# Kernel tuning notes

Hardware: AMD Instinct MI355X
Metric: run time of the kernel (lower is better)

The kernel has to match this reference:

```python
import jax, jax.numpy as jnp
import numpy as np

NU, NI, K, D, B = 100000, 50000, 100, 64, 8192


def setup_inputs() -> dict:
    key = jax.random.key(0)
    ks = jax.random.split(key, 16)
    s = lambda fan_in: np.sqrt(2.0 / fan_in)  # kaiming_normal-ish scale
    return {
        "user_emb": jax.random.normal(ks[0], (NU, D), jnp.float32) * s(D),
        "item_emb": jax.random.normal(ks[1], (NI, D), jnp.float32) * s(D),
        "user_scr_tensor": jax.random.uniform(ks[2], (NU, K), jnp.float32) / K,
        "item_scr_tensor": jax.random.uniform(ks[3], (NI, K), jnp.float32) / K,
        "w1": jax.random.normal(ks[4], (64, 128), jnp.float32) * s(128),
        "b1": jnp.zeros((64,), jnp.float32),
        "w2": jax.random.normal(ks[5], (64, 64), jnp.float32) * s(64),
        "b2": jnp.zeros((64,), jnp.float32),
        "w3": jax.random.normal(ks[6], (32, 64), jnp.float32) * s(64),
        "b3": jnp.zeros((32,), jnp.float32),
        "w4": jax.random.normal(ks[7], (32, 32), jnp.float32) * s(32),
        "b4": jnp.zeros((32,), jnp.float32),
        "w5": jax.random.normal(ks[8], (1, 32), jnp.float32) * s(32),
        "b5": jnp.zeros((1,), jnp.float32),
        "user_idx_tensor": jax.random.randint(ks[9], (NU, K), 0, NU, jnp.int32),
        "item_idx_tensor": jax.random.randint(ks[10], (NI, K), 0, NI, jnp.int32),
        "user_idxs": jax.random.randint(ks[11], (B,), 0, NU, jnp.int32),
        "item_idxs": jax.random.randint(ks[12], (B,), 0, NI, jnp.int32),
    }


def _scored_pool(idx_tensor, emb, scr, idxs):
    neighs = idx_tensor[idxs]          # [B, K]
    neigh_emb = emb[neighs]            # [B, K, D]
    neigh_scr = scr[neighs]            # [B, K, K]
    return jnp.einsum("bkj,bjd->bkd", neigh_scr, neigh_emb)


def reference(user_emb, item_emb, user_scr_tensor, item_scr_tensor,
              w1, b1, w2, b2, w3, b3, w4, b4, w5, b5,
              user_idx_tensor, item_idx_tensor, user_idxs, item_idxs):
    su = _scored_pool(user_idx_tensor, user_emb, user_scr_tensor, user_idxs)  # [B,K,D]
    si = _scored_pool(item_idx_tensor, item_emb, item_scr_tensor, item_idxs)  # [B,K,D]
    x = jnp.concatenate([su, si], axis=2)  # [B, K, 2D]
    x = jax.nn.relu(x @ w1.T + b1)
    x = jax.nn.relu(x @ w2.T + b2)
    x = jax.nn.relu(x @ w3.T + b3)
    x = jax.nn.relu(x @ w4.T + b4)
    x = jax.nn.sigmoid(x @ w5.T + b5)  # [B, K, 1]
    return jnp.mean(x, axis=-2).squeeze()  # [B]
```

## Files before the change

kernel.cpp:

```cpp
#include <hip/hip_runtime.h>
#include <hip/hip_bf16.h>
#include <math.h>

typedef __attribute__((ext_vector_type(8))) short short8;
typedef __attribute__((ext_vector_type(4))) float f32x4;

#define KN 100

#define W1_OFF 0
#define W2_OFF 8192
#define W3_OFF 12288
#define W4_OFF 14336
#define SCRU_OFF 16384
#define SCRI_OFF (SCRU_OFF + 100000 * 128)
#define EMBU_OFF (SCRI_OFF + 50000 * 128)
#define EMBI_OFF (EMBU_OFF + 100000 * 64)

#define ET_STRIDE 136
#define ETU_OFF 14336
#define ETI_OFF (14336 + 64 * ET_STRIDE)
#define S_TOT   (14336 + 2 * 64 * ET_STRIDE)

__device__ __forceinline__ unsigned short f2bf(float f) {
  __hip_bfloat16 h = __float2bfloat16(f);
  return __builtin_bit_cast(unsigned short, h);
}

__device__ __forceinline__ void st8(unsigned short* d, float4 a, float4 b) {
  short8 h;
  h[0] = (short)f2bf(a.x); h[1] = (short)f2bf(a.y);
  h[2] = (short)f2bf(a.z); h[3] = (short)f2bf(a.w);
  h[4] = (short)f2bf(b.x); h[5] = (short)f2bf(b.y);
  h[6] = (short)f2bf(b.z); h[7] = (short)f2bf(b.w);
  *reinterpret_cast<short8*>(d) = h;
}

__device__ __forceinline__ short8 pk2(f32x4 a, f32x4 b) {
  short8 h;
  h[0] = (short)f2bf(a[0]); h[1] = (short)f2bf(a[1]);
  h[2] = (short)f2bf(a[2]); h[3] = (short)f2bf(a[3]);
  h[4] = (short)f2bf(b[0]); h[5] = (short)f2bf(b[1]);
  h[6] = (short)f2bf(b[2]); h[7] = (short)f2bf(b[3]);
  return h;
}

#define PREP_UNITS (15360 + 2400000 + 1200000)
__global__ void prep(const float* __restrict__ w1, const float* __restrict__ w2,
                     const float* __restrict__ w3, const float* __restrict__ w4,
                     const float* __restrict__ uscr, const float* __restrict__ iscr,
                     const float* __restrict__ uemb, const float* __restrict__ iemb,
                     unsigned short* __restrict__ ws) {
  const float4 z4 = {0.f, 0.f, 0.f, 0.f};
  const int stride = gridDim.x * 256;
  for (int t = blockIdx.x * 256 + threadIdx.x; t < PREP_UNITS; t += stride) {
    if (t < 15360) {
      const float* src; int rel, o, i, kt, base;
      if (t < 8192)       { src = w1; rel = t;         o = rel >> 7; i = rel & 127; kt = 4; base = W1_OFF; }
      else if (t < 12288) { src = w2; rel = t - 8192;  o = rel >> 6; i = rel & 63;  kt = 2; base = W2_OFF; }
      else if (t < 14336) { src = w3; rel = t - 12288; o = rel >> 6; i = rel & 63;  kt = 2; base = W3_OFF; }
      else                { src = w4; rel = t - 14336; o = rel >> 5; i = rel & 31;  kt = 1; base = W4_OFF; }
      int n = o >> 4, l15 = o & 15, k = i >> 5;
      int quad = (i >> 2) & 3, s = ((i >> 4) & 1) * 4 + (i & 3);
      ws[base + ((n * kt + k) * 64 + quad * 16 + l15) * 8 + s] = f2bf(src[rel]);
      continue;
    }
    int rel = t - 15360;
    if (rel < 2400000) {
      const float* src; unsigned short* dst; int row, g;
      if (rel < 1600000) {
        row = rel >> 4; g = rel & 15;
        src = uscr + (size_t)row * 100;
        dst = ws + SCRU_OFF + (size_t)row * 128 + g * 8;
      } else {
        int q = rel - 1600000; row = q >> 4; g = q & 15;
        src = iscr + (size_t)row * 100;
        dst = ws + SCRI_OFF + (size_t)row * 128 + g * 8;
      }
      const int jb = 32 * (g >> 2) + 4 * (g & 3);
      float4 va = (jb <= 96) ? *reinterpret_cast<const float4*>(src + jb) : z4;
      float4 vb = (jb <= 80) ? *reinterpret_cast<const float4*>(src + jb + 16) : z4;
      st8(dst, va, vb);
      continue;
    }
    rel -= 2400000;
    {
      const float* src; unsigned short* dst; int row, g;
      if (rel < 800000) {
        row = rel >> 3; g = rel & 7;
        src = uemb + (size_t)row * 64;
        dst = ws + EMBU_OFF + (size_t)row * 64 + g * 8;
      } else {
        int q = rel - 800000; row = q >> 3; g = q & 7;
        src = iemb + (size_t)row * 64;
        dst = ws + EMBI_OFF + (size_t)row * 64 + g * 8;
      }
      float4 va = *reinterpret_cast<const float4*>(src + g * 8);
      float4 vb = *reinterpret_cast<const float4*>(src + g * 8 + 4);
      st8(dst, va, vb);
    }
  }
}

__device__ __forceinline__ void pool_mfma(const unsigned short* __restrict__ Sb,
                                          const short8* sb, int l15, int quad,
                                          short8& f0, short8& f1) {
  f32x4 acc[4];
#pragma unroll
  for (int po = 0; po < 4; ++po) acc[po] = (f32x4){0.f, 0.f, 0.f, 0.f};
#pragma unroll
  for (int k4 = 0; k4 < 4; ++k4) {
#pragma unroll
    for (int po = 0; po < 4; ++po) {
      const int row = po * 16 + l15;
      const int hw = row * ET_STRIDE + (((k4 * 4 + quad) ^ ((row >> 3) & 7)) << 3);
      short8 ea = *reinterpret_cast<const short8*>(Sb + hw);
      acc[po] = __builtin_amdgcn_mfma_f32_16x16x32_bf16(ea, sb[k4], acc[po], 0, 0, 0);
    }
  }
  f0 = pk2(acc[0], acc[1]);
  f1 = pk2(acc[2], acc[3]);
}

__device__ __forceinline__ void et_store(unsigned short* __restrict__ S,
                                         const unsigned int* ev, int w, int c,
                                         int half, int base) {
#pragma unroll
  for (int rr = 0; rr < 8; ++rr) {
    const int rbase = w + rr * 7;
    if (rbase < 50) {
      const int r0 = rbase * 2;
      const int p0 = ((r0 >> 5) << 5) | (((r0 >> 2) & 3) << 3) |
                     (((r0 >> 4) & 1) << 2) | (r0 & 3);
      const int sw = ((c >> 2) & 7) << 3;
      const int q = (2 * c + half) * ET_STRIDE + (p0 ^ sw);
      unsigned int v = ev[rr];
      unsigned int p = __shfl_xor(v, 32, 64);
      unsigned int d = half ? ((v & 0xffff0000u) | (p >> 16))
                            : ((v & 0x0000ffffu) | (p << 16));
      *reinterpret_cast<unsigned int*>(&S[base + q]) = d;
    }
  }
}

__launch_bounds__(448, 4)
__global__ void cnn_mfma9(
    const unsigned short* __restrict__ ws,
    const float* __restrict__ b1, const float* __restrict__ b2,
    const float* __restrict__ b3, const float* __restrict__ b4,
    const float* __restrict__ w5, const float* __restrict__ b5,
    const int* __restrict__ user_idx_t, const int* __restrict__ item_idx_t,
    const int* __restrict__ user_idxs, const int* __restrict__ item_idxs,
    float* __restrict__ out) {
  __shared__ __align__(16) unsigned short S[S_TOT];
  __shared__ float s_red[7];

  const int b = blockIdx.x;
  const int tid = threadIdx.x;
  const int w = tid >> 6;
  const int lane = tid & 63;
  const int l15 = lane & 15, quad = lane >> 4;
  const int mrow = w * 16 + l15;
  const int c = lane & 31, half = lane >> 5;

  short8 wtmp[4];
#pragma unroll
  for (int i = 0; i < 4; ++i)
    wtmp[i] = reinterpret_cast<const short8*>(ws)[tid + i * 448];

  const int ub = user_idxs[b] * KN;
  const int ibx = item_idxs[b] * KN;
  int nbu_s[8], nbi_s[8];
#pragma unroll
  for (int rr = 0; rr < 8; ++rr) {
    const int rbase = w + rr * 7;
    if (rbase < 50) {
      const int r = rbase * 2 + half;
      nbu_s[rr] = user_idx_t[ub + r];
      nbi_s[rr] = item_idx_t[ibx + r];
    } else {
      nbu_s[rr] = 0; nbi_s[rr] = 0;
    }
  }
  const int mr = (mrow < KN) ? mrow : 0;
  const int nbu_m = user_idx_t[ub + mr];
  const int nbi_m = item_idx_t[ibx + mr];

  unsigned int evu[8], evi[8];
#pragma unroll
  for (int rr = 0; rr < 8; ++rr) {
    const int rbase = w + rr * 7;
    if (rbase < 50) {
      evu[rr] = *reinterpret_cast<const unsigned int*>(
          ws + EMBU_OFF + (size_t)nbu_s[rr] * 64 + c * 2);
      evi[rr] = *reinterpret_cast<const unsigned int*>(
          ws + EMBI_OFF + (size_t)nbi_s[rr] * 64 + c * 2);
    } else {
      evu[rr] = 0u; evi[rr] = 0u;
    }
  }
  short8 sbu[4], sbi[4];
  {
    const unsigned short* arow = ws + SCRU_OFF + (size_t)nbu_m * 128;
#pragma unroll
    for (int k = 0; k < 4; ++k)
      sbu[k] = *reinterpret_cast<const short8*>(arow + k * 32 + quad * 8);
  }
  {
    const unsigned short* arow = ws + SCRI_OFF + (size_t)nbi_m * 128;
#pragma unroll
    for (int k = 0; k < 4; ++k)
      sbi[k] = *reinterpret_cast<const short8*>(arow + k * 32 + quad * 8);
  }

  {
    const short8 z8 = {0, 0, 0, 0, 0, 0, 0, 0};
    const uint2 z2 = {0u, 0u};
    for (int i = tid; i < 512; i += 448) {
      const int buf = i >> 8;
      const int rem = i & 255;
      const int row = rem >> 2, ci = rem & 3;
      const int sw = (row >> 3) & 7;
      const int base = (buf ? ETI_OFF : ETU_OFF) + row * ET_STRIDE;
      if (ci == 0) {
        *reinterpret_cast<uint2*>(&S[base + ((12 ^ sw) << 3) + 4]) = z2;
      } else {
        *reinterpret_cast<short8*>(&S[base + (((12 + ci) ^ sw) << 3)]) = z8;
      }
    }
  }

#pragma unroll
  for (int i = 0; i < 4; ++i)
    reinterpret_cast<short8*>(S)[tid + i * 448] = wtmp[i];
  et_store(S, evu, w, c, half, ETU_OFF);
  et_store(S, evi, w, c, half, ETI_OFF);
  __syncthreads();

  short8 x0, x1, x2, x3;
  pool_mfma(S + ETU_OFF, sbu, l15, quad, x0, x1);
  pool_mfma(S + ETI_OFF, sbi, l15, quad, x2, x3);

  f32x4 y[4];
#pragma unroll
  for (int po = 0; po < 4; ++po) y[po] = (f32x4){0.f, 0.f, 0.f, 0.f};
  {
    short8 xf[4] = {x0, x1, x2, x3};
#pragma unroll
    for (int k4 = 0; k4 < 4; ++k4)
#pragma unroll
      for (int po = 0; po < 4; ++po) {
        short8 wa = *reinterpret_cast<const short8*>(
            S + W1_OFF + ((po * 4 + k4) * 64 + lane) * 8);
        y[po] = __builtin_amdgcn_mfma_f32_16x16x32_bf16(wa, xf[k4], y[po], 0, 0, 0);
      }
  }
#pragma unroll
  for (int po = 0; po < 4; ++po) {
    const float4 bb = *reinterpret_cast<const float4*>(b1 + po * 16 + quad * 4);
#pragma unroll
    for (int r = 0; r < 4; ++r) y[po][r] = fmaxf(y[po][r] + bb[r], 0.f);
  }
  short8 g0 = pk2(y[0], y[1]), g1 = pk2(y[2], y[3]);

  f32x4 v[4];
#pragma unroll
  for (int po = 0; po < 4; ++po) v[po] = (f32x4){0.f, 0.f, 0.f, 0.f};
#pragma unroll
  for (int k4 = 0; k4 < 2; ++k4) {
    short8 gf = k4 ? g1 : g0;
#pragma unroll
    for (int po = 0; po < 4; ++po) {
      short8 wa = *reinterpret_cast<const short8*>(
          S + W2_OFF + ((po * 2 + k4) * 64 + lane) * 8);
      v[po] = __builtin_amdgcn_mfma_f32_16x16x32_bf16(wa, gf, v[po], 0, 0, 0);
    }
  }
#pragma unroll
  for (int po = 0; po < 4; ++po) {
    const float4 bb = *reinterpret_cast<const float4*>(b2 + po * 16 + quad * 4);
#pragma unroll
    for (int r = 0; r < 4; ++r) v[po][r] = fmaxf(v[po][r] + bb[r], 0.f);
  }
  short8 h0 = pk2(v[0], v[1]), h1 = pk2(v[2], v[3]);

  f32x4 t3[2];
  t3[0] = (f32x4){0.f, 0.f, 0.f, 0.f};
  t3[1] = (f32x4){0.f, 0.f, 0.f, 0.f};
#pragma unroll
  for (int k4 = 0; k4 < 2; ++k4) {
    short8 gf = k4 ? h1 : h0;
#pragma unroll
    for (int po = 0; po < 2; ++po) {
      short8 wa = *reinterpret_cast<const short8*>(
          S + W3_OFF + ((po * 2 + k4) * 64 + lane) * 8);
      t3[po] = __builtin_amdgcn_mfma_f32_16x16x32_bf16(wa, gf, t3[po], 0, 0, 0);
    }
  }
#pragma unroll
  for (int po = 0; po < 2; ++po) {
    const float4 bb = *reinterpret_cast<const float4*>(b3 + po * 16 + quad * 4);
#pragma unroll
    for (int r = 0; r < 4; ++r) t3[po][r] = fmaxf(t3[po][r] + bb[r], 0.f);
  }
  short8 q0 = pk2(t3[0], t3[1]);

  f32x4 u[2];
  u[0] = (f32x4){0.f, 0.f, 0.f, 0.f};
  u[1] = (f32x4){0.f, 0.f, 0.f, 0.f};
#pragma unroll
  for (int po = 0; po < 2; ++po) {
    short8 wa = *reinterpret_cast<const short8*>(ws + W4_OFF + (po * 64 + lane) * 8);
    u[po] = __builtin_amdgcn_mfma_f32_16x16x32_bf16(wa, q0, u[po], 0, 0, 0);
  }
  float part = 0.f;
#pragma unroll
  for (int po = 0; po < 2; ++po) {
    const float4 bb = *reinterpret_cast<const float4*>(b4 + po * 16 + quad * 4);
    const float4 wv = *reinterpret_cast<const float4*>(w5 + po * 16 + quad * 4);
#pragma unroll
    for (int r = 0; r < 4; ++r)
      part = fmaf(fmaxf(u[po][r] + bb[r], 0.f), wv[r], part);
  }
  part += __shfl_xor(part, 16, 64);
  part += __shfl_xor(part, 32, 64);
  float sig = 1.f / (1.f + expf(-(part + b5[0])));
  if (mrow >= KN) sig = 0.f;
  sig += __shfl_xor(sig, 1, 64);
  sig += __shfl_xor(sig, 2, 64);
  sig += __shfl_xor(sig, 4, 64);
  sig += __shfl_xor(sig, 8, 64);
  if (lane == 0) s_red[w] = sig;
  __syncthreads();
  if (tid == 0) {
    float acc = 0.f;
#pragma unroll
    for (int i = 0; i < 7; ++i) acc += s_red[i];
    out[b] = acc * (1.0f / KN);
  }
}

extern "C" void kernel_launch(void* const* d_in, const int* in_sizes, int n_in,
                              void* d_out, int out_size, void* d_ws,
                              size_t ws_size, hipStream_t stream) {
  const float* user_emb = (const float*)d_in[0];
  const float* item_emb = (const float*)d_in[1];
  const float* user_scr = (const float*)d_in[2];
  const float* item_scr = (const float*)d_in[3];
  const float* w1 = (const float*)d_in[4];
  const float* b1 = (const float*)d_in[5];
  const float* w2 = (const float*)d_in[6];
  const float* b2 = (const float*)d_in[7];
  const float* w3 = (const float*)d_in[8];
  const float* b3 = (const float*)d_in[9];
  const float* w4 = (const float*)d_in[10];
  const float* b4 = (const float*)d_in[11];
  const float* w5 = (const float*)d_in[12];
  const float* b5 = (const float*)d_in[13];
  const int* user_idx_t = (const int*)d_in[14];
  const int* item_idx_t = (const int*)d_in[15];
  const int* user_idxs = (const int*)d_in[16];
  const int* item_idxs = (const int*)d_in[17];
  unsigned short* wsw = (unsigned short*)d_ws;

  prep<<<dim3(2048), dim3(256), 0, stream>>>(
      w1, w2, w3, w4, user_scr, item_scr, user_emb, item_emb, wsw);

  const int B = in_sizes[16];
  cnn_mfma9<<<dim3(B), dim3(448), 0, stream>>>(
      wsw, b1, b2, b3, b4, w5, b5, user_idx_t, item_idx_t, user_idxs,
      item_idxs, (float*)d_out);
}
```

Before: 353.7 us.

## Process multiple batch rows per block with prefetched neighbor gathers

Each block now loops over 16 batch elements instead of one. Weights are staged into shared memory once per block, and the next element's neighbor indices and embedding rows are prefetched into registers while the current element's MLP runs. This amortizes weight staging and overlaps gather latency with compute. The cost is a much smaller grid, which reduces the number of resident blocks available to hide memory latency.

```diff
diff --git a/kernel.cpp b/kernel.cpp
--- a/kernel.cpp
+++ b/kernel.cpp
@@ -6,6 +6,7 @@
 typedef __attribute__((ext_vector_type(4))) float f32x4;
 
 #define KN 100
+#define ITERS 16
 
 #define W1_OFF 0
 #define W2_OFF 8192
@@ -142,19 +143,58 @@
   }
 }
 
+__device__ __forceinline__ void load_idx(
+    int b, int w, int half, int mrow,
+    const int* __restrict__ user_idx_t, const int* __restrict__ item_idx_t,
+    const int* __restrict__ user_idxs, const int* __restrict__ item_idxs,
+    int* nbu_e, int* nbi_e, int& nbu_m, int& nbi_m) {
+  const int ub = user_idxs[b] * KN;
+  const int ibx = item_idxs[b] * KN;
+#pragma unroll
+  for (int rr = 0; rr < 8; ++rr) {
+    const int rbase = w + rr * 7;
+    if (rbase < 50) {
+      const int r = rbase * 2 + half;
+      nbu_e[rr] = user_idx_t[ub + r];
+      nbi_e[rr] = item_idx_t[ibx + r];
+    } else {
+      nbu_e[rr] = 0; nbi_e[rr] = 0;
+    }
+  }
+  const int mr = (mrow < KN) ? mrow : 0;
+  nbu_m = user_idx_t[ub + mr];
+  nbi_m = item_idx_t[ibx + mr];
+}
+
+__device__ __forceinline__ void gather_emb(
+    const unsigned short* __restrict__ ws, int w, int c,
+    const int* nbu_e, const int* nbi_e, unsigned int* evu, unsigned int* evi) {
+#pragma unroll
+  for (int rr = 0; rr < 8; ++rr) {
+    const int rbase = w + rr * 7;
+    if (rbase < 50) {
+      evu[rr] = *reinterpret_cast<const unsigned int*>(
+          ws + EMBU_OFF + (size_t)nbu_e[rr] * 64 + c * 2);
+      evi[rr] = *reinterpret_cast<const unsigned int*>(
+          ws + EMBI_OFF + (size_t)nbi_e[rr] * 64 + c * 2);
+    } else {
+      evu[rr] = 0u; evi[rr] = 0u;
+    }
+  }
+}
+
 __launch_bounds__(448, 4)
-__global__ void cnn_mfma9(
+__global__ void cnn_mfma10(
     const unsigned short* __restrict__ ws,
     const float* __restrict__ b1, const float* __restrict__ b2,
     const float* __restrict__ b3, const float* __restrict__ b4,
     const float* __restrict__ w5, const float* __restrict__ b5,
     const int* __restrict__ user_idx_t, const int* __restrict__ item_idx_t,
     const int* __restrict__ user_idxs, const int* __restrict__ item_idxs,
-    float* __restrict__ out) {
+    float* __restrict__ out, int B) {
   __shared__ __align__(16) unsigned short S[S_TOT];
   __shared__ float s_red[7];
 
-  const int b = blockIdx.x;
   const int tid = threadIdx.x;
   const int w = tid >> 6;
   const int lane = tid & 63;
@@ -162,56 +202,14 @@
   const int mrow = w * 16 + l15;
   const int c = lane & 31, half = lane >> 5;
 
+  const int bbase = blockIdx.x * ITERS;
+  const int nit = (B - bbase < ITERS) ? (B - bbase) : ITERS;
+  if (nit <= 0) return;
+
   short8 wtmp[4];
 #pragma unroll
   for (int i = 0; i < 4; ++i)
     wtmp[i] = reinterpret_cast<const short8*>(ws)[tid + i * 448];
-
-  const int ub = user_idxs[b] * KN;
-  const int ibx = item_idxs[b] * KN;
-  int nbu_s[8], nbi_s[8];
-#pragma unroll
-  for (int rr = 0; rr < 8; ++rr) {
-    const int rbase = w + rr * 7;
-    if (rbase < 50) {
-      const int r = rbase * 2 + half;
-      nbu_s[rr] = user_idx_t[ub + r];
-      nbi_s[rr] = item_idx_t[ibx + r];
-    } else {
-      nbu_s[rr] = 0; nbi_s[rr] = 0;
-    }
-  }
-  const int mr = (mrow < KN) ? mrow : 0;
-  const int nbu_m = user_idx_t[ub + mr];
-  const int nbi_m = item_idx_t[ibx + mr];
-
-  unsigned int evu[8], evi[8];
-#pragma unroll
-  for (int rr = 0; rr < 8; ++rr) {
-    const int rbase = w + rr * 7;
-    if (rbase < 50) {
-      evu[rr] = *reinterpret_cast<const unsigned int*>(
-          ws + EMBU_OFF + (size_t)nbu_s[rr] * 64 + c * 2);
-      evi[rr] = *reinterpret_cast<const unsigned int*>(
-          ws + EMBI_OFF + (size_t)nbi_s[rr] * 64 + c * 2);
-    } else {
-      evu[rr] = 0u; evi[rr] = 0u;
-    }
-  }
-  short8 sbu[4], sbi[4];
-  {
-    const unsigned short* arow = ws + SCRU_OFF + (size_t)nbu_m * 128;
-#pragma unroll
-    for (int k = 0; k < 4; ++k)
-      sbu[k] = *reinterpret_cast<const short8*>(arow + k * 32 + quad * 8);
-  }
-  {
-    const unsigned short* arow = ws + SCRI_OFF + (size_t)nbi_m * 128;
-#pragma unroll
-    for (int k = 0; k < 4; ++k)
-      sbi[k] = *reinterpret_cast<const short8*>(arow + k * 32 + quad * 8);
-  }
-
   {
     const short8 z8 = {0, 0, 0, 0, 0, 0, 0, 0};
     const uint2 z2 = {0u, 0u};
@@ -228,114 +226,144 @@
       }
     }
   }
-
 #pragma unroll
   for (int i = 0; i < 4; ++i)
     reinterpret_cast<short8*>(S)[tid + i * 448] = wtmp[i];
-  et_store(S, evu, w, c, half, ETU_OFF);
-  et_store(S, evi, w, c, half, ETI_OFF);
-  __syncthreads();
-
-  short8 x0, x1, x2, x3;
-  pool_mfma(S + ETU_OFF, sbu, l15, quad, x0, x1);
-  pool_mfma(S + ETI_OFF, sbi, l15, quad, x2, x3);
-
-  f32x4 y[4];
-#pragma unroll
-  for (int po = 0; po < 4; ++po) y[po] = (f32x4){0.f, 0.f, 0.f, 0.f};
-  {
-    short8 xf[4] = {x0, x1, x2, x3};
-#pragma unroll
-    for (int k4 = 0; k4 < 4; ++k4)
+
+  int nbu_e[8], nbi_e[8], nbu_m, nbi_m;
+  unsigned int evu[8], evi[8];
+  load_idx(bbase, w, half, mrow, user_idx_t, item_idx_t, user_idxs, item_idxs,
+           nbu_e, nbi_e, nbu_m, nbi_m);
+  gather_emb(ws, w, c, nbu_e, nbi_e, evu, evi);
+
+  for (int it = 0; it < nit; ++it) {
+    const int b = bbase + it;
+
+    short8 sbu[4], sbi[4];
+    {
+      const unsigned short* arow = ws + SCRU_OFF + (size_t)nbu_m * 128;
+#pragma unroll
+      for (int k = 0; k < 4; ++k)
+        sbu[k] = *reinterpret_cast<const short8*>(arow + k * 32 + quad * 8);
+    }
+    {
+      const unsigned short* arow = ws + SCRI_OFF + (size_t)nbi_m * 128;
+#pragma unroll
+      for (int k = 0; k < 4; ++k)
+        sbi[k] = *reinterpret_cast<const short8*>(arow + k * 32 + quad * 8);
+    }
+
+    et_store(S, evu, w, c, half, ETU_OFF);
+    et_store(S, evi, w, c, half, ETI_OFF);
+    __syncthreads();
+
+    short8 x0, x1, x2, x3;
+    pool_mfma(S + ETU_OFF, sbu, l15, quad, x0, x1);
+    pool_mfma(S + ETI_OFF, sbi, l15, quad, x2, x3);
+
+    if (it + 1 < nit) {
+      load_idx(b + 1, w, half, mrow, user_idx_t, item_idx_t, user_idxs,
+               item_idxs, nbu_e, nbi_e, nbu_m, nbi_m);
+      gather_emb(ws, w, c, nbu_e, nbi_e, evu, evi);
+    }
+
+    f32x4 y[4];
+#pragma unroll
+    for (int po = 0; po < 4; ++po) y[po] = (f32x4){0.f, 0.f, 0.f, 0.f};
+    {
+      short8 xf[4] = {x0, x1, x2, x3};
+#pragma unroll
+      for (int k4 = 0; k4 < 4; ++k4)
+#pragma unroll
+        for (int po = 0; po < 4; ++po) {
+          short8 wa = *reinterpret_cast<const short8*>(
+              S + W1_OFF + ((po * 4 + k4) * 64 + lane) * 8);
+          y[po] = __builtin_amdgcn_mfma_f32_16x16x32_bf16(wa, xf[k4], y[po], 0, 0, 0);
+        }
+    }
+#pragma unroll
+    for (int po = 0; po < 4; ++po) {
+      const float4 bb = *reinterpret_cast<const float4*>(b1 + po * 16 + quad * 4);
+#pragma unroll
+      for (int r = 0; r < 4; ++r) y[po][r] = fmaxf(y[po][r] + bb[r], 0.f);
+    }
+    short8 g0 = pk2(y[0], y[1]), g1 = pk2(y[2], y[3]);
+
+    f32x4 v[4];
+#pragma unroll
+    for (int po = 0; po < 4; ++po) v[po] = (f32x4){0.f, 0.f, 0.f, 0.f};
+#pragma unroll
+    for (int k4 = 0; k4 < 2; ++k4) {
+      short8 gf = k4 ? g1 : g0;
 #pragma unroll
       for (int po = 0; po < 4; ++po) {
         short8 wa = *reinterpret_cast<const short8*>(
-            S + W1_OFF + ((po * 4 + k4) * 64 + lane) * 8);
-        y[po] = __builtin_amdgcn_mfma_f32_16x16x32_bf16(wa, xf[k4], y[po], 0, 0, 0);
+            S + W2_OFF + ((po * 2 + k4) * 64 + lane) * 8);
+        v[po] = __builtin_amdgcn_mfma_f32_16x16x32_bf16(wa, gf, v[po], 0, 0, 0);
       }
-  }
-#pragma unroll
-  for (int po = 0; po < 4; ++po) {
-    const float4 bb = *reinterpret_cast<const float4*>(b1 + po * 16 + quad * 4);
-#pragma unroll
-    for (int r = 0; r < 4; ++r) y[po][r] = fmaxf(y[po][r] + bb[r], 0.f);
-  }
-  short8 g0 = pk2(y[0], y[1]), g1 = pk2(y[2], y[3]);
-
-  f32x4 v[4];
-#pragma unroll
-  for (int po = 0; po < 4; ++po) v[po] = (f32x4){0.f, 0.f, 0.f, 0.f};
-#pragma unroll
-  for (int k4 = 0; k4 < 2; ++k4) {
-    short8 gf = k4 ? g1 : g0;
+    }
 #pragma unroll
     for (int po = 0; po < 4; ++po) {
-      short8 wa = *reinterpret_cast<const short8*>(
-          S + W2_OFF + ((po * 2 + k4) * 64 + lane) * 8);
-      v[po] = __builtin_amdgcn_mfma_f32_16x16x32_bf16(wa, gf, v[po], 0, 0, 0);
-    }
-  }
-#pragma unroll
-  for (int po = 0; po < 4; ++po) {
-    const float4 bb = *reinterpret_cast<const float4*>(b2 + po * 16 + quad * 4);
-#pragma unroll
-    for (int r = 0; r < 4; ++r) v[po][r] = fmaxf(v[po][r] + bb[r], 0.f);
-  }
-  short8 h0 = pk2(v[0], v[1]), h1 = pk2(v[2], v[3]);
-
-  f32x4 t3[2];
-  t3[0] = (f32x4){0.f, 0.f, 0.f, 0.f};
-  t3[1] = (f32x4){0.f, 0.f, 0.f, 0.f};
-#pragma unroll
-  for (int k4 = 0; k4 < 2; ++k4) {
-    short8 gf = k4 ? h1 : h0;
+      const float4 bb = *reinterpret_cast<const float4*>(b2 + po * 16 + quad * 4);
+#pragma unroll
+      for (int r = 0; r < 4; ++r) v[po][r] = fmaxf(v[po][r] + bb[r], 0.f);
+    }
+    short8 h0 = pk2(v[0], v[1]), h1 = pk2(v[2], v[3]);
+
+    f32x4 t3[2];
+    t3[0] = (f32x4){0.f, 0.f, 0.f, 0.f};
+    t3[1] = (f32x4){0.f, 0.f, 0.f, 0.f};
+#pragma unroll
+    for (int k4 = 0; k4 < 2; ++k4) {
+      short8 gf = k4 ? h1 : h0;
+#pragma unroll
+      for (int po = 0; po < 2; ++po) {
+        short8 wa = *reinterpret_cast<const short8*>(
+            S + W3_OFF + ((po * 2 + k4) * 64 + lane) * 8);
+        t3[po] = __builtin_amdgcn_mfma_f32_16x16x32_bf16(wa, gf, t3[po], 0, 0, 0);
+      }
+    }
 #pragma unroll
     for (int po = 0; po < 2; ++po) {
-      short8 wa = *reinterpret_cast<const short8*>(
-          S + W3_OFF + ((po * 2 + k4) * 64 + lane) * 8);
-      t3[po] = __builtin_amdgcn_mfma_f32_16x16x32_bf16(wa, gf, t3[po], 0, 0, 0);
-    }
-  }
-#pragma unroll
-  for (int po = 0; po < 2; ++po) {
-    const float4 bb = *reinterpret_cast<const float4*>(b3 + po * 16 + quad * 4);
-#pragma unroll
-    for (int r = 0; r < 4; ++r) t3[po][r] = fmaxf(t3[po][r] + bb[r], 0.f);
-  }
-  short8 q0 = pk2(t3[0], t3[1]);
-
-  f32x4 u[2];
-  u[0] = (f32x4){0.f, 0.f, 0.f, 0.f};
-  u[1] = (f32x4){0.f, 0.f, 0.f, 0.f};
-#pragma unroll
-  for (int po = 0; po < 2; ++po) {
-    short8 wa = *reinterpret_cast<const short8*>(ws + W4_OFF + (po * 64 + lane) * 8);
-    u[po] = __builtin_amdgcn_mfma_f32_16x16x32_bf16(wa, q0, u[po], 0, 0, 0);
-  }
-  float part = 0.f;
-#pragma unroll
-  for (int po = 0; po < 2; ++po) {
-    const float4 bb = *reinterpret_cast<const float4*>(b4 + po * 16 + quad * 4);
-    const float4 wv = *reinterpret_cast<const float4*>(w5 + po * 16 + quad * 4);
-#pragma unroll
-    for (int r = 0; r < 4; ++r)
-      part = fmaf(fmaxf(u[po][r] + bb[r], 0.f), wv[r], part);
-  }
-  part += __shfl_xor(part, 16, 64);
-  part += __shfl_xor(part, 32, 64);
-  float sig = 1.f / (1.f + expf(-(part + b5[0])));
-  if (mrow >= KN) sig = 0.f;
-  sig += __shfl_xor(sig, 1, 64);
-  sig += __shfl_xor(sig, 2, 64);
-  sig += __shfl_xor(sig, 4, 64);
-  sig += __shfl_xor(sig, 8, 64);
-  if (lane == 0) s_red[w] = sig;
-  __syncthreads();
-  if (tid == 0) {
-    float acc = 0.f;
-#pragma unroll
-    for (int i = 0; i < 7; ++i) acc += s_red[i];
-    out[b] = acc * (1.0f / KN);
+      const float4 bb = *reinterpret_cast<const float4*>(b3 + po * 16 + quad * 4);
+#pragma unroll
+      for (int r = 0; r < 4; ++r) t3[po][r] = fmaxf(t3[po][r] + bb[r], 0.f);
+    }
+    short8 q0 = pk2(t3[0], t3[1]);
+
+    f32x4 u[2];
+    u[0] = (f32x4){0.f, 0.f, 0.f, 0.f};
+    u[1] = (f32x4){0.f, 0.f, 0.f, 0.f};
+#pragma unroll
+    for (int po = 0; po < 2; ++po) {
+      short8 wa = *reinterpret_cast<const short8*>(ws + W4_OFF + (po * 64 + lane) * 8);
+      u[po] = __builtin_amdgcn_mfma_f32_16x16x32_bf16(wa, q0, u[po], 0, 0, 0);
+    }
+    float part = 0.f;
+#pragma unroll
+    for (int po = 0; po < 2; ++po) {
+      const float4 bb = *reinterpret_cast<const float4*>(b4 + po * 16 + quad * 4);
+      const float4 wv = *reinterpret_cast<const float4*>(w5 + po * 16 + quad * 4);
+#pragma unroll
+      for (int r = 0; r < 4; ++r)
+        part = fmaf(fmaxf(u[po][r] + bb[r], 0.f), wv[r], part);
+    }
+    part += __shfl_xor(part, 16, 64);
+    part += __shfl_xor(part, 32, 64);
+    float sig = 1.f / (1.f + expf(-(part + b5[0])));
+    if (mrow >= KN) sig = 0.f;
+    sig += __shfl_xor(sig, 1, 64);
+    sig += __shfl_xor(sig, 2, 64);
+    sig += __shfl_xor(sig, 4, 64);
+    sig += __shfl_xor(sig, 8, 64);
+    if (lane == 0) s_red[w] = sig;
+    __syncthreads();
+    if (tid == 0) {
+      float acc = 0.f;
+#pragma unroll
+      for (int i = 0; i < 7; ++i) acc += s_red[i];
+      out[b] = acc * (1.0f / KN);
+    }
   }
 }
 
@@ -366,7 +394,8 @@
       w1, w2, w3, w4, user_scr, item_scr, user_emb, item_emb, wsw);
 
   const int B = in_sizes[16];
-  cnn_mfma9<<<dim3(B), dim3(448), 0, stream>>>(
+  const int nblk = (B + ITERS - 1) / ITERS;
+  cnn_mfma10<<<dim3(nblk), dim3(448), 0, stream>>>(
       wsw, b1, b2, b3, b4, w5, b5, user_idx_t, item_idx_t, user_idxs,
-      item_idxs, (float*)d_out);
-}
+      item_idxs, (float*)d_out, B);
+}
```

After: 840.0 us. +137.5%, slower.
